# Optimization experiments

Measured on AMD Instinct MI355X. Metric: run time of the kernel, lower is better.

## Reference

```python
import jax, jax.numpy as jnp
import numpy as np

N_DELAYS = 512
N_SAMPLES = 2 ** 15  # 32768


def _interp_linear(x, out_size):
    # F.interpolate(mode='linear', align_corners=False) on [B, C, L]
    L = x.shape[-1]
    scale = L / out_size
    pos = (jnp.arange(out_size, dtype=jnp.float32) + 0.5) * scale - 0.5
    pos = jnp.clip(pos, 0.0, L - 1)
    i0 = jnp.floor(pos).astype(jnp.int32)
    i1 = jnp.minimum(i0 + 1, L - 1)
    w = (pos - i0).astype(x.dtype)
    return x[..., i0] * (1.0 - w) + x[..., i1] * w


def _interp_nearest(x, out_size):
    # F.interpolate(mode='nearest') on [B, C, L]: idx = floor(j * L/out)
    L = x.shape[-1]
    idx = jnp.clip(jnp.floor(jnp.arange(out_size) * (L / out_size)).astype(jnp.int32), 0, L - 1)
    return x[..., idx]


def setup_inputs() -> dict:
    key = jax.random.key(0)
    k1, k2, k3, k4, k5 = jax.random.split(key, 5)
    batch = 8
    impulse = jax.random.normal(k1, (batch, 128), dtype=jnp.float32)
    delay_selection = jax.random.normal(k2, (batch, N_DELAYS, 16), dtype=jnp.float32)
    damping = jax.random.normal(k3, (batch, 1), dtype=jnp.float32)
    filt = jax.random.normal(k4, (batch, 16), dtype=jnp.float32)
    # torch forward draws uniform(-1,1) noise; passed as input for determinism
    noise = jax.random.uniform(k5, (batch, 1, N_SAMPLES), dtype=jnp.float32, minval=-1.0, maxval=1.0)
    # comb-filter buffer: delays[i, ::i+1] = 1
    delays_np = np.zeros((N_DELAYS, N_SAMPLES), dtype=np.float32)
    for i in range(N_DELAYS):
        delays_np[i, ::i + 1] = 1.0
    delays = jnp.asarray(delays_np)
    return {"impulse": impulse, "delay_selection": delay_selection, "damping": damping,
            "filt": filt, "noise": noise, "delays": delays}


def reference(impulse, delay_selection, damping, filt, noise, delays):
    batch = delay_selection.shape[0]
    n_delays, n_samples = delays.shape
    n_frames = filt.shape[-1]

    # filter spectrum envelope: sigmoid -> linear upsample to n_samples//2 -> pad 1
    f = jax.nn.sigmoid(filt).reshape(-1, 1, n_frames)
    f = _interp_linear(f, n_samples // 2)
    filt_spec = jnp.pad(f, ((0, 0), (0, 0), (0, 1)))  # [B,1,n_samples//2+1]

    # impulse: squared envelope upsampled, modulating uniform noise
    imp = impulse.reshape(batch, 1, -1) ** 2
    imp = _interp_linear(imp, n_samples) * noise  # [B,1,n_samples]

    # damping: powers = linspace(1, 1, n_frames) == ones (faithful to source)
    damp = jax.nn.sigmoid(damping.reshape(batch, 1)) * 0.9999
    powers = jnp.linspace(1.0, float(damp.shape[-1]), n_frames)
    damp = damp[:, :, None] ** powers[None, None, :]  # [B,1,n_frames]
    damp = _interp_nearest(damp, n_samples)  # [B,1,n_samples]

    # sparse comb selection: softmax over delays, nearest upsample, weighted sum
    ds = jax.nn.softmax(delay_selection.reshape(batch, n_delays, -1), axis=1)
    ds = _interp_nearest(ds, n_samples)  # [B,n_delays,n_samples]
    d = jnp.einsum('bdn,dn->bn', ds, delays)[:, None, :] * damp  # [B,1,n_samples]

    # FFT convolution
    delay_spec = jnp.fft.rfft(d, axis=-1, norm='ortho')
    impulse_spec = jnp.fft.rfft(imp, axis=-1, norm='ortho')
    spec = delay_spec * impulse_spec * filt_spec
    final = jnp.fft.irfft(spec, n=n_samples, axis=-1, norm='ortho')
    return final
```

## Files before the change

### kernel.cpp

```cpp
#include <hip/hip_runtime.h>
#include <math.h>

#define NSAMP 32768
#define NDEL  512
#define NFR   16
#define BATCH 8
#define TWO_PI 6.283185307179586f

__device__ __forceinline__ float2 cmul(float2 a, float2 b) {
    return make_float2(a.x*b.x - a.y*b.y, a.x*b.y + a.y*b.x);
}
__device__ __forceinline__ float2 cadd(float2 a, float2 b){ return make_float2(a.x+b.x, a.y+b.y); }
__device__ __forceinline__ float2 csub(float2 a, float2 b){ return make_float2(a.x-b.x, a.y-b.y); }
__device__ __forceinline__ float2 crot(float2 z, float sign){ return make_float2(-sign*z.y, sign*z.x); }

__device__ __forceinline__ int phi(int i){ return i + (i >> 3); }

__device__ __forceinline__ void bfly8(const float2 v[8], float sign, float2 X[8]) {
    const float S2 = 0.70710678118654752f;
    float2 t0 = cadd(v[0], v[4]), t1 = csub(v[0], v[4]);
    float2 t2 = cadd(v[2], v[6]), t3 = crot(csub(v[2], v[6]), sign);
    float2 E0 = cadd(t0, t2), E1 = cadd(t1, t3), E2 = csub(t0, t2), E3 = csub(t1, t3);
    float2 u0 = cadd(v[1], v[5]), u1 = csub(v[1], v[5]);
    float2 u2 = cadd(v[3], v[7]), u3 = crot(csub(v[3], v[7]), sign);
    float2 O0 = cadd(u0, u2), O1 = cadd(u1, u3), O2 = csub(u0, u2), O3 = csub(u1, u3);
    float2 c1 = make_float2( S2, sign*S2);
    float2 c3 = make_float2(-S2, sign*S2);
    float2 w1o = cmul(c1, O1);
    float2 w2o = crot(O2, sign);
    float2 w3o = cmul(c3, O3);
    X[0]=cadd(E0,O0);  X[4]=csub(E0,O0);
    X[1]=cadd(E1,w1o); X[5]=csub(E1,w1o);
    X[2]=cadd(E2,w2o); X[6]=csub(E2,w2o);
    X[3]=cadd(E3,w3o); X[7]=csub(E3,w3o);
}

__device__ __forceinline__ void twiddle_q(float2 v[8], float ang1) {
    float sa, ca; __sincosf(ang1, &sa, &ca);
    float2 w1 = make_float2(ca, sa), wq = w1;
#pragma unroll
    for (int q = 1; q < 8; ++q) { v[q] = cmul(v[q], wq); wq = cmul(wq, w1); }
}

__global__ void build_kernel(const float* __restrict__ impulse,
                             const float* __restrict__ dsel,
                             const float* __restrict__ damping,
                             const float* __restrict__ noise,
                             float2* __restrict__ A) {
    const int b   = blockIdx.x >> 6;
    const int f   = (blockIdx.x >> 2) & 15;
    const int sub = blockIdx.x & 3;
    const int tid = threadIdx.x;
    __shared__ float Wrow[NDEL];
    __shared__ float dl[512];
    __shared__ float red[64];

    float v[8], m = -1e30f;
#pragma unroll
    for (int k = 0; k < 8; ++k) {
        v[k] = dsel[(b*NDEL + tid + 64*k)*NFR + f];
        m = fmaxf(m, v[k]);
    }
    red[tid] = m;
    __syncthreads();
    for (int off = 32; off > 0; off >>= 1) {
        if (tid < off) red[tid] = fmaxf(red[tid], red[tid+off]);
        __syncthreads();
    }
    float M = red[0];
    __syncthreads();
    float e[8], s = 0.0f;
#pragma unroll
    for (int k = 0; k < 8; ++k) { e[k] = expf(v[k] - M); s += e[k]; }
    red[tid] = s;
    __syncthreads();
    for (int off = 32; off > 0; off >>= 1) {
        if (tid < off) red[tid] += red[tid+off];
        __syncthreads();
    }
    float S = red[0];
    float damp = 1.0f/(1.0f + expf(-damping[b])) * 0.9999f;
    float scale = damp / S;
#pragma unroll
    for (int k = 0; k < 8; ++k) Wrow[tid + 64*k] = e[k] * scale;
    for (int k = tid; k < 512; k += 64) dl[k] = 0.0f;
    __syncthreads();

    const unsigned start = ((unsigned)f << 11) + ((unsigned)sub << 9);
    const float fstart = (float)start;

    for (unsigned t = 1; t < 64; ++t) {
        float wt = Wrow[t-1];
        unsigned q0 = (unsigned)(__fdividef(fstart, (float)t));
        unsigned n0 = q0 * t;
        while (n0 < start) n0 += t;
        while (n0 >= start + t) n0 -= t;
        for (unsigned i = (n0 - start) + (unsigned)tid * t; i < 512u; i += 64u * t)
            atomicAdd(&dl[i], wt);
    }
    for (unsigned t = 64u + (unsigned)tid; t <= 512u; t += 64u) {
        float wt = Wrow[t-1];
        unsigned q0 = (unsigned)(__fdividef(fstart, (float)t));
        unsigned n0 = q0 * t;
        while (n0 < start) n0 += t;
        while (n0 >= start + t) n0 -= t;
        for (unsigned i = n0 - start; i < 512u; i += t)
            atomicAdd(&dl[i], wt);
    }
    __syncthreads();

    for (int k = tid; k < 512; k += 64) {
        int n = (int)start + k;
        float pos = (n + 0.5f) * (1.0f/256.0f) - 0.5f;
        pos = fminf(fmaxf(pos, 0.0f), 127.0f);
        int i0 = (int)pos;
        float w = pos - (float)i0;
        int i1 = (i0 + 1 > 127) ? 127 : i0 + 1;
        float x0 = impulse[b*128 + i0]; x0 *= x0;
        float x1 = impulse[b*128 + i1]; x1 *= x1;
        float iv = (x0*(1.0f - w) + x1*w) * noise[b*NSAMP + n];
        A[b*NSAMP + n] = make_float2(dl[k], iv);
    }
}

__global__ void fft512_kernel(const float2* __restrict__ src,
                              float2* __restrict__ dst,
                              const float* __restrict__ filt,
                              float sign) {
    const int j  = threadIdx.x;
    const int s  = blockIdx.x >> 6;
    const int n2 = blockIdx.x & 63;
    __shared__ float2 buf[2][576];
    __shared__ float fs[NFR];
    if (filt && j < NFR)
        fs[j] = 1.0f/(1.0f + expf(-filt[s*NFR + j]));
    __syncthreads();

    const float2* sp = src + s * NSAMP;
    float2 v[8], X[8];
    if (!filt) {
#pragma unroll
        for (int q = 0; q < 8; ++q) v[q] = sp[64*j + 4096*q + n2];
    } else {
        const float SCALE = 1.0f / (32768.0f * 181.01933598375618f);
#pragma unroll
        for (int q = 0; q < 8; ++q) {
            int m = 64*j + 4096*q + n2;
            float2 Zk = sp[m];
            float2 Zr = sp[(NSAMP - m) & (NSAMP - 1)];
            float2 Zrc = make_float2(Zr.x, -Zr.y);
            float2 D = make_float2(0.5f*(Zk.x + Zrc.x), 0.5f*(Zk.y + Zrc.y));
            float2 df = make_float2(Zk.x - Zrc.x, Zk.y - Zrc.y);
            float2 I = make_float2(0.5f*df.y, -0.5f*df.x);
            int jjb = (m <= NSAMP - m) ? m : NSAMP - m;
            float fv = 0.0f;
            if (jjb < NSAMP/2) {
                float pos = (jjb + 0.5f) * (1.0f/1024.0f) - 0.5f;
                pos = fminf(fmaxf(pos, 0.0f), 15.0f);
                int i0 = (int)pos;
                float w = pos - (float)i0;
                int i1 = (i0 + 1 > 15) ? 15 : i0 + 1;
                fv = fs[i0]*(1.0f - w) + fs[i1]*w;
            }
            float2 spc = cmul(D, I);
            float g = fv * SCALE;
            v[q] = make_float2(spc.x * g, spc.y * g);
        }
    }

    bfly8(v, sign, X);
#pragma unroll
    for (int r = 0; r < 8; ++r) buf[0][phi(8*j + r)] = X[r];
    __syncthreads();
#pragma unroll
    for (int q = 0; q < 8; ++q) v[q] = buf[0][phi(j + 64*q)];
    int jm = j & 7;
    twiddle_q(v, sign * TWO_PI * (float)jm * (1.0f/64.0f));
    bfly8(v, sign, X);
#pragma unroll
    for (int r = 0; r < 8; ++r) buf[1][phi(((j>>3)<<6) + jm + (r<<3))] = X[r];
    __syncthreads();
#pragma unroll
    for (int q = 0; q < 8; ++q) v[q] = buf[1][phi(j + 64*q)];
    twiddle_q(v, sign * TWO_PI * (float)j * (1.0f/512.0f));
    bfly8(v, sign, X);

    float2* dp = dst + s * NSAMP + n2 * 512;
#pragma unroll
    for (int r = 0; r < 8; ++r) {
        int k1 = j + 64*r;
        int pr = (n2 * k1) & (NSAMP - 1);
        float sa, ca; __sincosf(sign * TWO_PI * (float)pr * (1.0f/32768.0f), &sa, &ca);
        dp[k1] = cmul(X[r], make_float2(ca, sa));
    }
}

__global__ void fft64_kernel(const float2* __restrict__ src,
                             float2* __restrict__ dst,
                             float* __restrict__ out_real,
                             float sign) {
    const int l = threadIdx.x;
    const int c = l & 7, jj = l >> 3;
    const int s = blockIdx.x >> 6;
    const int k1base = (blockIdx.x & 63) << 3;
    __shared__ float2 buf[576];

    const float2* sp = src + s * NSAMP;
    float2 v[8], X[8];
#pragma unroll
    for (int q = 0; q < 8; ++q) v[q] = sp[(jj + 8*q)*512 + k1base + c];

    bfly8(v, sign, X);
#pragma unroll
    for (int r = 0; r < 8; ++r) buf[phi(c*64 + jj*8 + r)] = X[r];
    __syncthreads();
#pragma unroll
    for (int q = 0; q < 8; ++q) v[q] = buf[phi(c*64 + jj + 8*q)];
    twiddle_q(v, sign * TWO_PI * (float)jj * (1.0f/64.0f));
    bfly8(v, sign, X);

    int base = s * NSAMP + k1base + c;
    if (out_real) {
#pragma unroll
        for (int r = 0; r < 8; ++r) out_real[base + 512*(jj + 8*r)] = X[r].x;
    } else {
#pragma unroll
        for (int r = 0; r < 8; ++r) dst[base + 512*(jj + 8*r)] = X[r];
    }
}

extern "C" void kernel_launch(void* const* d_in, const int* in_sizes, int n_in,
                              void* d_out, int out_size, void* d_ws, size_t ws_size,
                              hipStream_t stream) {
    const float* impulse = (const float*)d_in[0];
    const float* dsel    = (const float*)d_in[1];
    const float* damping = (const float*)d_in[2];
    const float* filt    = (const float*)d_in[3];
    const float* noise   = (const float*)d_in[4];
    float* out = (float*)d_out;

    float2* A = (float2*)d_ws;
    float2* B = A + BATCH * NSAMP;

    build_kernel<<<dim3(512), dim3(64), 0, stream>>>(impulse, dsel, damping, noise, A);
    fft512_kernel<<<dim3(512), dim3(64), 0, stream>>>(A, B, nullptr, -1.0f);
    fft64_kernel <<<dim3(512), dim3(64), 0, stream>>>(B, A, nullptr, -1.0f);
    fft512_kernel<<<dim3(512), dim3(64), 0, stream>>>(A, B, filt, 1.0f);
    fft64_kernel <<<dim3(512), dim3(64), 0, stream>>>(B, nullptr, out, 1.0f);
}
```

Baseline: 143.2 us.

## Store intermediate FFT buffers transposed so fft512 loads are contiguous

```diff
diff --git a/kernel.cpp b/kernel.cpp
--- a/kernel.cpp
+++ b/kernel.cpp
@@ -46,7 +46,7 @@
                              const float* __restrict__ dsel,
                              const float* __restrict__ damping,
                              const float* __restrict__ noise,
-                             float2* __restrict__ A) {
+                             float2* __restrict__ At) {
     const int b   = blockIdx.x >> 6;
     const int f   = (blockIdx.x >> 2) & 15;
     const int sub = blockIdx.x & 3;
@@ -109,8 +109,11 @@
     }
     __syncthreads();
 
-    for (int k = tid; k < 512; k += 64) {
-        int n = (int)start + k;
+    const int n1base = (int)(start >> 6);
+    float2* op = At + b*NSAMP + tid*512 + n1base;
+#pragma unroll
+    for (int q = 0; q < 8; ++q) {
+        int n = (int)start + tid + 64*q;
         float pos = (n + 0.5f) * (1.0f/256.0f) - 0.5f;
         pos = fminf(fmaxf(pos, 0.0f), 127.0f);
         int i0 = (int)pos;
@@ -119,7 +122,7 @@
         float x0 = impulse[b*128 + i0]; x0 *= x0;
         float x1 = impulse[b*128 + i1]; x1 *= x1;
         float iv = (x0*(1.0f - w) + x1*w) * noise[b*NSAMP + n];
-        A[b*NSAMP + n] = make_float2(dl[k], iv);
+        op[q] = make_float2(dl[tid + 64*q], iv);
     }
 }
 
@@ -140,14 +143,17 @@
     float2 v[8], X[8];
     if (!filt) {
 #pragma unroll
-        for (int q = 0; q < 8; ++q) v[q] = sp[64*j + 4096*q + n2];
+        for (int q = 0; q < 8; ++q) v[q] = sp[n2*512 + j + 64*q];
     } else {
         const float SCALE = 1.0f / (32768.0f * 181.01933598375618f);
+        const int prow = (64 - n2) & 63;
 #pragma unroll
         for (int q = 0; q < 8; ++q) {
-            int m = 64*j + 4096*q + n2;
-            float2 Zk = sp[m];
-            float2 Zr = sp[(NSAMP - m) & (NSAMP - 1)];
+            int n1 = j + 64*q;
+            int m  = 64*n1 + n2;
+            float2 Zk = sp[n2*512 + n1];
+            int pcol = n2 ? (511 - n1) : ((512 - n1) & 511);
+            float2 Zr = sp[prow*512 + pcol];
             float2 Zrc = make_float2(Zr.x, -Zr.y);
             float2 D = make_float2(0.5f*(Zk.x + Zrc.x), 0.5f*(Zk.y + Zrc.y));
             float2 df = make_float2(Zk.x - Zrc.x, Zk.y - Zrc.y);
@@ -196,7 +202,7 @@
 }
 
 __global__ void fft64_kernel(const float2* __restrict__ src,
-                             float2* __restrict__ dst,
+                             float2* __restrict__ dstT,
                              float* __restrict__ out_real,
                              float sign) {
     const int l = threadIdx.x;
@@ -219,13 +225,15 @@
     twiddle_q(v, sign * TWO_PI * (float)jj * (1.0f/64.0f));
     bfly8(v, sign, X);
 
-    int base = s * NSAMP + k1base + c;
+    const int k1 = k1base + c;
     if (out_real) {
-#pragma unroll
-        for (int r = 0; r < 8; ++r) out_real[base + 512*(jj + 8*r)] = X[r].x;
+        float* op = out_real + s * NSAMP + k1;
+#pragma unroll
+        for (int r = 0; r < 8; ++r) op[512*(jj + 8*r)] = X[r].x;
     } else {
-#pragma unroll
-        for (int r = 0; r < 8; ++r) dst[base + 512*(jj + 8*r)] = X[r];
+        float2* dp = dstT + s * NSAMP + (k1 & 63)*512 + (k1 >> 6) + 8*jj;
+#pragma unroll
+        for (int r = 0; r < 8; ++r) dp[64*r] = X[r];
     }
 }
 
```

Result: faster. 135.9 us (median of 2 runs) (-5.1%).
